# Performance work log

Measured on AMD Instinct MI355X. Metric: run time of the kernel, lower is better.

## Reference

```python
import jax, jax.numpy as jnp
import numpy as np

N_HEAD = 16
ROPE_BASE = 10000.0


def rope_cache(T, dim):
    half = dim // 2
    inv_freq = 1.0 / (ROPE_BASE ** (jnp.arange(half, dtype=jnp.float32) / half))
    freqs = jnp.arange(T, dtype=jnp.float32)[:, None] * inv_freq[None, :]  # [T, half]
    cos = jnp.repeat(jnp.cos(freqs), 2, axis=-1)  # [T, dim]
    sin = jnp.repeat(jnp.sin(freqs), 2, axis=-1)
    return cos, sin


def apply_rope(x, cos, sin):
    # x: [B, H, T, hd]; cos/sin: [T, hd] broadcast over B,H
    x1 = x[..., ::2]
    x2 = x[..., 1::2]
    x_rot = jnp.stack([-x2, x1], axis=-1).reshape(x.shape)
    return x * cos + x_rot * sin


def setup_inputs() -> dict:
    key = jax.random.key(0)
    k1, k2, k3, k4 = jax.random.split(key, 4)
    C = 1024
    x = jax.random.normal(k1, (2, 2048, C), jnp.float32)
    w_qkv = jax.random.normal(k2, (3 * C, C), jnp.float32) * 0.02
    w_out = jax.random.normal(k3, (C, C), jnp.float32) * 0.02
    b_out = jax.random.normal(k4, (C,), jnp.float32) * 0.02
    return {"x": x, "w_qkv": w_qkv, "w_out": w_out, "b_out": b_out}


def reference(x, w_qkv, w_out, b_out):
    B, T, C = x.shape
    H = N_HEAD
    hd = C // H
    qkv = x @ w_qkv.T                              # [B, T, 3C]
    qkv = qkv.reshape(B, T, 3, H, hd).transpose(2, 0, 3, 1, 4)  # [3, B, H, T, hd]
    q, k, v = qkv[0], qkv[1], qkv[2]
    cos, sin = rope_cache(T, hd)
    q = apply_rope(q, cos, sin)
    k = apply_rope(k, cos, sin)
    scale = hd ** (-0.5)
    scores = jnp.einsum('bhqd,bhkd->bhqk', q, k) * scale       # [B, H, T, T]
    causal = jnp.tril(jnp.ones((T, T), dtype=bool))
    scores = jnp.where(causal, scores, jnp.float32(-jnp.inf))
    att = jax.nn.softmax(scores, axis=-1)
    out = jnp.einsum('bhqk,bhkd->bhqd', att, v)                # [B, H, T, hd]
    out = out.transpose(0, 2, 1, 3).reshape(B, T, C)
    return out @ w_out.T + b_out
```

## Files before the change

kernel.cpp:

```cpp
#include <hip/hip_runtime.h>
#include <math.h>

namespace {

typedef __attribute__((ext_vector_type(8))) short s16x8;
typedef __attribute__((ext_vector_type(4))) float f32x4;
typedef unsigned int u32;
typedef unsigned short u16;

constexpr int B_ = 2;
constexpr int T_ = 2048;
constexpr int C_ = 1024;
constexpr int H_ = 16;
constexpr float L2E = 1.44269504088896340736f;

__device__ inline u16 f2bf(float x) {
    __bf16 h = (__bf16)x;
    return __builtin_bit_cast(u16, h);
}
__device__ inline u32 packbf2(float a, float b) {
    return (u32)f2bf(a) | ((u32)f2bf(b) << 16);
}
__device__ inline void gload_lds16(const void* g, void* lds) {
    __builtin_amdgcn_global_load_lds(
        (const __attribute__((address_space(1))) unsigned int*)g,
        (__attribute__((address_space(3))) unsigned int*)lds, 16, 0, 0);
}

__global__ __launch_bounds__(256) void tab_k(float2* __restrict__ cs) {
    int idx = blockIdx.x * 256 + threadIdx.x;
    int t = idx >> 5, i = idx & 31;
    float inv = 1.0f / powf(10000.0f, (float)i / 32.0f);
    float ang = (float)t * inv;
    cs[idx] = make_float2(cosf(ang), sinf(ang));
}

__global__ __launch_bounds__(256)
void cvt_k(const float4* __restrict__ x, const float4* __restrict__ wq,
           const float4* __restrict__ wo, uint2* __restrict__ xb,
           uint2* __restrict__ wqb, uint2* __restrict__ wob) {
    int i = blockIdx.x * 256 + threadIdx.x;
    const float4* s;
    uint2* d;
    int j;
    if (i < 1048576) { s = x; d = xb; j = i; }
    else if (i < 1048576 + 786432) { s = wq; d = wqb; j = i - 1048576; }
    else { s = wo; d = wob; j = i - (1048576 + 786432); }
    float4 v = s[j];
    d[j] = make_uint2(packbf2(v.x, v.y), packbf2(v.z, v.w));
}

__global__ __launch_bounds__(256)
void qkv_mfma_k(const u16* __restrict__ xb, const u16* __restrict__ wqb,
                const float2* __restrict__ cs, u16* __restrict__ qb,
                u16* __restrict__ kb, u16* __restrict__ vt) {
    __shared__ char lds[32768];
    const int tid = threadIdx.x;
    const int w = tid >> 6, lane = tid & 63;
    const int c = lane & 15, g = lane >> 4;
    const int n0 = blockIdx.x * 128, m0 = blockIdx.y * 128;
    const int wr = w >> 1, wc = w & 1;

    f32x4 acc[4][4];
#pragma unroll
    for (int i = 0; i < 4; ++i)
#pragma unroll
        for (int j = 0; j < 4; ++j) acc[i][j] = (f32x4){0.f, 0.f, 0.f, 0.f};

    const u16* Ab = xb + (size_t)m0 * C_;
    const u16* Bb = wqb + (size_t)n0 * C_;
    const int srow = tid >> 2, sslot = tid & 3;

    auto stage = [&](int k0, char* base) {
#pragma unroll
        for (int call = 0; call < 2; ++call) {
            int r = call * 64 + srow;
            int ds = sslot ^ ((r >> 1) & 3);
            gload_lds16(Ab + (size_t)r * C_ + k0 + ds * 8, base + call * 4096 + w * 1024);
            gload_lds16(Bb + (size_t)r * C_ + k0 + ds * 8, base + 8192 + call * 4096 + w * 1024);
        }
    };
    auto compute = [&](const char* base) {
        s16x8 aF[4], bF[4];
#pragma unroll
        for (int mf = 0; mf < 4; ++mf) {
            int row = wr * 64 + mf * 16 + c;
            aF[mf] = *(const s16x8*)(base + row * 64 + ((g ^ ((row >> 1) & 3)) * 16));
        }
#pragma unroll
        for (int nf = 0; nf < 4; ++nf) {
            int row = wc * 64 + nf * 16 + c;
            bF[nf] = *(const s16x8*)(base + 8192 + row * 64 + ((g ^ ((row >> 1) & 3)) * 16));
        }
#pragma unroll
        for (int mf = 0; mf < 4; ++mf)
#pragma unroll
            for (int nf = 0; nf < 4; ++nf)
                acc[mf][nf] = __builtin_amdgcn_mfma_f32_16x16x32_bf16(aF[mf], bF[nf], acc[mf][nf], 0, 0, 0);
    };

    stage(0, lds);
    __syncthreads();
    int cur = 0;
    for (int t = 0; t < 31; ++t) {
        stage((t + 1) * 32, lds + ((cur ^ 1) << 14));
        compute(lds + (cur << 14));
        __syncthreads();
        cur ^= 1;
    }
    compute(lds + (cur << 14));

    const int sec = n0 >> 10;
    const int h = ((n0 & 1023) >> 6) + wc;
    const int b = m0 >> 11;
    const int t0w = (m0 & 2047) + wr * 64;
    const int bh = b * H_ + h;
    if (sec < 2) {
        u16* dst = (sec == 0) ? qb : kb;
        const float qs = (sec == 0) ? 0.125f : 1.0f;
#pragma unroll
        for (int nf = 0; nf < 4; ++nf) {
            int d = nf * 16 + c;
            int ibase = nf * 8 + (c >> 1);
#pragma unroll
            for (int mf = 0; mf < 4; ++mf) {
#pragma unroll
                for (int r = 0; r < 4; ++r) {
                    int t = t0w + mf * 16 + g * 4 + r;
                    float own = acc[mf][nf][r];
                    float partner = __shfl_xor(own, 1);
                    float2 csv = cs[t * 32 + ibase];
                    float rot = (d & 1) ? (own * csv.x + partner * csv.y)
                                        : (own * csv.x - partner * csv.y);
                    rot *= qs;
                    float rothi = __shfl_xor(rot, 1);
                    if (!(d & 1))
                        *(u32*)(dst + ((size_t)bh * T_ + t) * 64 + d) = packbf2(rot, rothi);
                }
            }
        }
    } else {
#pragma unroll
        for (int nf = 0; nf < 4; ++nf) {
            int d = nf * 16 + c;
#pragma unroll
            for (int mf = 0; mf < 4; ++mf) {
                int tb = t0w + mf * 16 + g * 4;
                u32 lo = packbf2(acc[mf][nf][0], acc[mf][nf][1]);
                u32 hi = packbf2(acc[mf][nf][2], acc[mf][nf][3]);
                *(uint2*)(vt + ((size_t)bh * 64 + d) * T_ + tb) = make_uint2(lo, hi);
            }
        }
    }
}

__global__ __launch_bounds__(256)
void flash_mfma_k(const u16* __restrict__ qb, const u16* __restrict__ kb,
                  const u16* __restrict__ vt, u16* __restrict__ attb) {
    __shared__ char lds[32768];
    char* Qs = lds;
    char* Ks = lds + 8192;
    char* Vs = lds + 16384;
    char* Ps = lds + 24576;
    const int tid = threadIdx.x, w = tid >> 6, lane = tid & 63;
    const int c = lane & 15, g = lane >> 4;
    const int bh = blockIdx.x;
    const int qi = 31 - blockIdx.y;
    const int q0 = qi * 64, q0w = q0 + w * 16;
    const u16* Qg = qb + ((size_t)bh * T_ + q0) * 64;
    const u16* Kg = kb + (size_t)bh * T_ * 64;
    const u16* Vg = vt + (size_t)bh * 64 * T_;

#pragma unroll
    for (int call = 0; call < 2; ++call) {
        int row = call * 32 + (tid >> 3);
        int ds = (tid & 7) ^ (row & 7);
        gload_lds16(Qg + (size_t)row * 64 + ds * 8, Qs + call * 4096 + w * 1024);
    }
    __syncthreads();

    s16x8 bQ[2];
#pragma unroll
    for (int kc = 0; kc < 2; ++kc) {
        int row = w * 16 + c;
        bQ[kc] = *(const s16x8*)(Qs + row * 128 + (((kc * 4 + g) ^ (row & 7)) * 16));
    }

    float m_ = -INFINITY, l_ = 0.f;
    f32x4 accO[4];
#pragma unroll
    for (int j = 0; j < 4; ++j) accO[j] = (f32x4){0.f, 0.f, 0.f, 0.f};

    const int nt = qi + 1;
    for (int kt = 0; kt < nt; ++kt) {
        __syncthreads();
        {
            int row = tid >> 3, slot = tid & 7;
#pragma unroll
            for (int call = 0; call < 2; ++call) {
                int r = call * 32 + row;
                int ds = slot ^ (r & 7);
                gload_lds16(Kg + (size_t)(kt * 64 + r) * 64 + ds * 8, Ks + call * 4096 + w * 1024);
                gload_lds16(Vg + (size_t)r * T_ + kt * 64 + ds * 8, Vs + call * 4096 + w * 1024);
            }
        }
        __syncthreads();

        f32x4 S[4];
#pragma unroll
        for (int mf = 0; mf < 4; ++mf) S[mf] = (f32x4){0.f, 0.f, 0.f, 0.f};
        s16x8 aK[4][2];
#pragma unroll
        for (int mf = 0; mf < 4; ++mf)
#pragma unroll
            for (int kc = 0; kc < 2; ++kc) {
                int row = mf * 16 + c;
                aK[mf][kc] = *(const s16x8*)(Ks + row * 128 + (((kc * 4 + g) ^ (row & 7)) * 16));
            }
#pragma unroll
        for (int kc = 0; kc < 2; ++kc)
#pragma unroll
            for (int mf = 0; mf < 4; ++mf)
                S[mf] = __builtin_amdgcn_mfma_f32_16x16x32_bf16(aK[mf][kc], bQ[kc], S[mf], 0, 0, 0);

        if (kt == qi) {
#pragma unroll
            for (int mf = 0; mf < 4; ++mf)
#pragma unroll
                for (int r = 0; r < 4; ++r) {
                    int kvg = kt * 64 + mf * 16 + g * 4 + r;
                    if (kvg > q0w + c) S[mf][r] = -INFINITY;
                }
        }

        float mx = -INFINITY;
#pragma unroll
        for (int mf = 0; mf < 4; ++mf)
#pragma unroll
            for (int r = 0; r < 4; ++r) mx = fmaxf(mx, S[mf][r]);
        mx = fmaxf(mx, __shfl_xor(mx, 16));
        mx = fmaxf(mx, __shfl_xor(mx, 32));
        float alpha = 1.0f;
        if (!__all(mx - m_ <= 8.0f)) {
            float mnew = fmaxf(m_, mx);
            alpha = exp2f((m_ - mnew) * L2E);
            m_ = mnew;
#pragma unroll
            for (int r = 0; r < 4; ++r) {
                float ar = __shfl(alpha, g * 4 + r);
#pragma unroll
                for (int nd = 0; nd < 4; ++nd) accO[nd][r] *= ar;
            }
        }
        float sum = 0.f;
#pragma unroll
        for (int mf = 0; mf < 4; ++mf)
#pragma unroll
            for (int r = 0; r < 4; ++r) {
                float p = exp2f((S[mf][r] - m_) * L2E);
                S[mf][r] = p;
                sum += p;
            }
        sum += __shfl_xor(sum, 16);
        sum += __shfl_xor(sum, 32);
        l_ = l_ * alpha + sum;

#pragma unroll
        for (int mf = 0; mf < 4; ++mf)
#pragma unroll
            for (int p2 = 0; p2 < 2; ++p2) {
                u32 v = packbf2(S[mf][2 * p2], S[mf][2 * p2 + 1]);
                int off = (mf * 16 + g * 4 + p2 * 2) * 2;
                *(u32*)(Ps + w * 2048 + c * 128 + (off ^ ((c & 7) << 4))) = v;
            }
        __threadfence_block();

        s16x8 aP[2], bV[4][2];
#pragma unroll
        for (int kc = 0; kc < 2; ++kc)
            aP[kc] = *(const s16x8*)(Ps + w * 2048 + c * 128 + (((kc * 4 + g) ^ (c & 7)) * 16));
#pragma unroll
        for (int nd = 0; nd < 4; ++nd)
#pragma unroll
            for (int kc = 0; kc < 2; ++kc) {
                int row = nd * 16 + c;
                bV[nd][kc] = *(const s16x8*)(Vs + row * 128 + (((kc * 4 + g) ^ (row & 7)) * 16));
            }
#pragma unroll
        for (int kc = 0; kc < 2; ++kc)
#pragma unroll
            for (int nd = 0; nd < 4; ++nd)
                accO[nd] = __builtin_amdgcn_mfma_f32_16x16x32_bf16(aP[kc], bV[nd][kc], accO[nd], 0, 0, 0);
    }

    const int hh = bh & 15;
    const int bb = bh >> 4;
#pragma unroll
    for (int r = 0; r < 4; ++r) {
        float linv = 1.0f / __shfl(l_, g * 4 + r);
        int t = q0w + g * 4 + r;
        size_t rowb = ((size_t)bb * T_ + t) * C_ + hh * 64;
#pragma unroll
        for (int nd = 0; nd < 4; ++nd)
            attb[rowb + nd * 16 + c] = f2bf(accO[nd][r] * linv);
    }
}

__global__ __launch_bounds__(256)
void proj_mfma_k(const u16* __restrict__ attb, const u16* __restrict__ wob,
                 const float* __restrict__ bias, float* __restrict__ out) {
    __shared__ char lds[32768];
    const int tid = threadIdx.x;
    const int w = tid >> 6, lane = tid & 63;
    const int c = lane & 15, g = lane >> 4;
    const int n0 = blockIdx.x * 128, m0 = blockIdx.y * 128;
    const int wr = w >> 1, wc = w & 1;

    f32x4 acc[4][4];
#pragma unroll
    for (int i = 0; i < 4; ++i)
#pragma unroll
        for (int j = 0; j < 4; ++j) acc[i][j] = (f32x4){0.f, 0.f, 0.f, 0.f};

    const u16* Ab = attb + (size_t)m0 * C_;
    const u16* Bb = wob + (size_t)n0 * C_;
    const int srow = tid >> 2, sslot = tid & 3;

    auto stage = [&](int k0, char* base) {
#pragma unroll
        for (int call = 0; call < 2; ++call) {
            int r = call * 64 + srow;
            int ds = sslot ^ ((r >> 1) & 3);
            gload_lds16(Ab + (size_t)r * C_ + k0 + ds * 8, base + call * 4096 + w * 1024);
            gload_lds16(Bb + (size_t)r * C_ + k0 + ds * 8, base + 8192 + call * 4096 + w * 1024);
        }
    };
    auto compute = [&](const char* base) {
        s16x8 aF[4], bF[4];
#pragma unroll
        for (int mf = 0; mf < 4; ++mf) {
            int row = wr * 64 + mf * 16 + c;
            aF[mf] = *(const s16x8*)(base + row * 64 + ((g ^ ((row >> 1) & 3)) * 16));
        }
#pragma unroll
        for (int nf = 0; nf < 4; ++nf) {
            int row = wc * 64 + nf * 16 + c;
            bF[nf] = *(const s16x8*)(base + 8192 + row * 64 + ((g ^ ((row >> 1) & 3)) * 16));
        }
#pragma unroll
        for (int mf = 0; mf < 4; ++mf)
#pragma unroll
            for (int nf = 0; nf < 4; ++nf)
                acc[mf][nf] = __builtin_amdgcn_mfma_f32_16x16x32_bf16(aF[mf], bF[nf], acc[mf][nf], 0, 0, 0);
    };

    stage(0, lds);
    __syncthreads();
    int cur = 0;
    for (int t = 0; t < 31; ++t) {
        stage((t + 1) * 32, lds + ((cur ^ 1) << 14));
        compute(lds + (cur << 14));
        __syncthreads();
        cur ^= 1;
    }
    compute(lds + (cur << 14));

#pragma unroll
    for (int nf = 0; nf < 4; ++nf) {
        int n = n0 + wc * 64 + nf * 16 + c;
        float bv = bias[n];
#pragma unroll
        for (int mf = 0; mf < 4; ++mf)
#pragma unroll
            for (int r = 0; r < 4; ++r) {
                int mrow = m0 + wr * 64 + mf * 16 + g * 4 + r;
                out[(size_t)mrow * C_ + n] = acc[mf][nf][r] + bv;
            }
    }
}

}

extern "C" void kernel_launch(void* const* d_in, const int* in_sizes, int n_in,
                              void* d_out, int out_size, void* d_ws, size_t ws_size,
                              hipStream_t stream) {
    const float* x     = (const float*)d_in[0];
    const float* w_qkv = (const float*)d_in[1];
    const float* w_out = (const float*)d_in[2];
    const float* b_out = (const float*)d_in[3];
    float* out = (float*)d_out;

    char* ws = (char*)d_ws;
    float2* cs = (float2*)ws;
    u16* xb   = (u16*)(ws + 524288);
    u16* wqb  = (u16*)(ws + 524288 + 8388608);
    u16* wob  = (u16*)(ws + 524288 + 8388608 + 6291456);
    u16* qb   = (u16*)(ws + 17301504);
    u16* kb   = (u16*)(ws + 25690112);
    u16* vt   = (u16*)(ws + 34078720);
    u16* attb = (u16*)(ws + 42467328);

    tab_k<<<256, 256, 0, stream>>>(cs);
    cvt_k<<<8192, 256, 0, stream>>>((const float4*)x, (const float4*)w_qkv,
                                    (const float4*)w_out, (uint2*)xb, (uint2*)wqb, (uint2*)wob);
    qkv_mfma_k<<<dim3(24, 32), 256, 0, stream>>>(xb, wqb, cs, qb, kb, vt);
    flash_mfma_k<<<dim3(32, 32), 256, 0, stream>>>(qb, kb, vt, attb);
    proj_mfma_k<<<dim3(8, 32), 256, 0, stream>>>(attb, wob, b_out, out);
}
```

Measured before the change: 224.0 us.

## Triple-buffer LDS staging in QKV and projection GEMMs with explicit waitcnt

Both bf16 MFMA GEMM kernels move from a double-buffered LDS pipeline with __syncthreads to a three-buffer ring. Each iteration waits with an explicit vmcnt so two global-to-LDS loads stay in flight, then issues a raw s_barrier. This lets a load run two k-steps ahead, hiding more global-memory latency. In exchange LDS use rises to 48KB per block, which may lower occupancy, and correctness now depends on hand-written waitcnt counts.

New measurement: 204.5 us. 1.1x faster.

```diff
diff --git a/kernel.cpp b/kernel.cpp
--- a/kernel.cpp
+++ b/kernel.cpp
@@ -26,6 +26,10 @@
         (const __attribute__((address_space(1))) unsigned int*)g,
         (__attribute__((address_space(3))) unsigned int*)lds, 16, 0, 0);
 }
+
+#define VMW(n) asm volatile("s_waitcnt vmcnt(" #n ")" ::: "memory")
+#define LGW0() asm volatile("s_waitcnt lgkmcnt(0)" ::: "memory")
+#define BARRIER() do { __builtin_amdgcn_s_barrier(); asm volatile("" ::: "memory"); } while (0)
 
 __global__ __launch_bounds__(256) void tab_k(float2* __restrict__ cs) {
     int idx = blockIdx.x * 256 + threadIdx.x;
@@ -54,7 +58,10 @@
 void qkv_mfma_k(const u16* __restrict__ xb, const u16* __restrict__ wqb,
                 const float2* __restrict__ cs, u16* __restrict__ qb,
                 u16* __restrict__ kb, u16* __restrict__ vt) {
-    __shared__ char lds[32768];
+    __shared__ char lds[49152];
+    char* const b0 = lds;
+    char* const b1 = lds + 16384;
+    char* const b2 = lds + 32768;
     const int tid = threadIdx.x;
     const int w = tid >> 6, lane = tid & 63;
     const int c = lane & 15, g = lane >> 4;
@@ -71,7 +78,8 @@
     const u16* Bb = wqb + (size_t)n0 * C_;
     const int srow = tid >> 2, sslot = tid & 3;
 
-    auto stage = [&](int k0, char* base) {
+    auto stage = [&](int t, char* base) {
+        int k0 = t * 32;
 #pragma unroll
         for (int call = 0; call < 2; ++call) {
             int r = call * 64 + srow;
@@ -99,16 +107,16 @@
                 acc[mf][nf] = __builtin_amdgcn_mfma_f32_16x16x32_bf16(aF[mf], bF[nf], acc[mf][nf], 0, 0, 0);
     };
 
-    stage(0, lds);
-    __syncthreads();
-    int cur = 0;
-    for (int t = 0; t < 31; ++t) {
-        stage((t + 1) * 32, lds + ((cur ^ 1) << 14));
-        compute(lds + (cur << 14));
-        __syncthreads();
-        cur ^= 1;
-    }
-    compute(lds + (cur << 14));
+    stage(0, b0);
+    stage(1, b1);
+#pragma unroll 1
+    for (int t = 0; t < 30; t += 3) {
+        VMW(4); BARRIER(); stage(t + 2, b2); compute(b0); LGW0();
+        VMW(4); BARRIER(); stage(t + 3, b0); compute(b1); LGW0();
+        VMW(4); BARRIER(); stage(t + 4, b1); compute(b2); LGW0();
+    }
+    VMW(4); BARRIER(); compute(b0); LGW0();
+    VMW(0); BARRIER(); compute(b1);
 
     const int sec = n0 >> 10;
     const int h = ((n0 & 1023) >> 6) + wc;
@@ -309,7 +317,10 @@
 __global__ __launch_bounds__(256)
 void proj_mfma_k(const u16* __restrict__ attb, const u16* __restrict__ wob,
                  const float* __restrict__ bias, float* __restrict__ out) {
-    __shared__ char lds[32768];
+    __shared__ char lds[49152];
+    char* const b0 = lds;
+    char* const b1 = lds + 16384;
+    char* const b2 = lds + 32768;
     const int tid = threadIdx.x;
     const int w = tid >> 6, lane = tid & 63;
     const int c = lane & 15, g = lane >> 4;
@@ -326,7 +337,8 @@
     const u16* Bb = wob + (size_t)n0 * C_;
     const int srow = tid >> 2, sslot = tid & 3;
 
-    auto stage = [&](int k0, char* base) {
+    auto stage = [&](int t, char* base) {
+        int k0 = t * 32;
 #pragma unroll
         for (int call = 0; call < 2; ++call) {
             int r = call * 64 + srow;
@@ -354,16 +366,16 @@
                 acc[mf][nf] = __builtin_amdgcn_mfma_f32_16x16x32_bf16(aF[mf], bF[nf], acc[mf][nf], 0, 0, 0);
     };
 
-    stage(0, lds);
-    __syncthreads();
-    int cur = 0;
-    for (int t = 0; t < 31; ++t) {
-        stage((t + 1) * 32, lds + ((cur ^ 1) << 14));
-        compute(lds + (cur << 14));
-        __syncthreads();
-        cur ^= 1;
-    }
-    compute(lds + (cur << 14));
+    stage(0, b0);
+    stage(1, b1);
+#pragma unroll 1
+    for (int t = 0; t < 30; t += 3) {
+        VMW(4); BARRIER(); stage(t + 2, b2); compute(b0); LGW0();
+        VMW(4); BARRIER(); stage(t + 3, b0); compute(b1); LGW0();
+        VMW(4); BARRIER(); stage(t + 4, b1); compute(b2); LGW0();
+    }
+    VMW(4); BARRIER(); compute(b0); LGW0();
+    VMW(0); BARRIER(); compute(b1);
 
 #pragma unroll
     for (int nf = 0; nf < 4; ++nf) {
```
